# Kernel optimization log

Measured on AMD Instinct MI355X. Metric: run time of the kernel, lower is better.

## Reference

```python
import jax, jax.numpy as jnp
import numpy as np

K = 3          # kernel_size
G = 4          # num_groups


def conv_same(x, w, b):
    # x: [B,H,W,Cin], w: [kh,kw,Cin,Cout] (HWIO)
    return jax.lax.conv_general_dilated(
        x, w, (1, 1), 'SAME', dimension_numbers=('NHWC', 'HWIO', 'NHWC')) + b


def depthwise_same(x, w, b):
    # w: [kh,kw,1,C], feature_group_count=C -> depthwise conv
    c = x.shape[-1]
    return jax.lax.conv_general_dilated(
        x, w, (1, 1), 'SAME', dimension_numbers=('NHWC', 'HWIO', 'NHWC'),
        feature_group_count=c) + b


def kernel_grid(k, dtype):
    off = (k - 1) / 2.0
    lin = jnp.linspace(-off, off, k).astype(dtype)
    xg, yg = jnp.meshgrid(lin, lin)            # default 'xy' indexing, as in TF
    return jnp.stack([xg, yg], axis=-1).reshape(-1, 2)   # [K*K, 2]


def sample_with_offsets(x, offsets, k):
    # x: [B,H,W,C], offsets: [B,H,W,2*k*k]
    B, H, W, C = x.shape
    dt = x.dtype
    gy, gx = jnp.meshgrid(jnp.arange(H, dtype=dt), jnp.arange(W, dtype=dt), indexing='ij')
    grid = jnp.stack([gx, gy], axis=-1)[None, :, :, None, :]      # [1,H,W,1,2] (x,y)
    off = offsets.reshape(B, H, W, k * k, 2)
    kg = kernel_grid(k, dt).reshape(1, 1, 1, k * k, 2)
    loc = grid + kg + off                                          # [B,H,W,K2,2]
    lx = jnp.clip(loc[..., 0], 0.0, W - 1.0)
    ly = jnp.clip(loc[..., 1], 0.0, H - 1.0)
    x0 = jnp.clip(jnp.floor(lx), 0.0, W - 1.0)
    y0 = jnp.clip(jnp.floor(ly), 0.0, H - 1.0)
    x1 = jnp.clip(x0 + 1.0, 0.0, W - 1.0)
    y1 = jnp.clip(y0 + 1.0, 0.0, H - 1.0)
    # bilinear weights (computed with clipped corner coords, exactly as the TF code)
    wa = (x1 - lx) * (y1 - ly)
    wb = (x1 - lx) * (ly - y0)
    wc = (lx - x0) * (y1 - ly)
    wd = (lx - x0) * (ly - y0)
    flat = x.reshape(B, H * W, C)
    N = H * W * k * k

    def gather(yi, xi):
        idx = (yi * W + xi).astype(jnp.int32).reshape(B, N)
        return jnp.take_along_axis(flat, idx[..., None], axis=1)   # [B,N,C]

    Ia = gather(y0, x0)
    Ib = gather(y1, x0)
    Ic = gather(y0, x1)
    Id = gather(y1, x1)
    w_ = lambda w: w.reshape(B, N, 1)
    interp = w_(wa) * Ia + w_(wb) * Ib + w_(wc) * Ic + w_(wd) * Id  # [B,N,C]
    return interp.reshape(B, H, W, k * k * C)


def setup_inputs() -> dict:
    key = jax.random.key(0)
    ks = jax.random.split(key, 6)
    B, H, W, C = 4, 96, 96, 256
    Cg = C // G                 # 64
    K2C = K * K * Cg            # 576
    GF = 256 // G               # group_filters = 64
    x = jax.random.normal(ks[0], (B, H, W, C), dtype=jnp.float32)
    w_init = jax.random.normal(ks[1], (1, 1, C, C), dtype=jnp.float32) / np.sqrt(C)
    b_init = jnp.zeros((C,), dtype=jnp.float32)
    # offset conv weights small so learned offsets stay within a few pixels
    w_off = jax.random.normal(ks[2], (G, K, K, Cg, 2 * K * K), dtype=jnp.float32) * 0.01
    b_off = jnp.zeros((G, 2 * K * K), dtype=jnp.float32)
    w_dw = jax.random.normal(ks[3], (G, K, K, 1, K2C), dtype=jnp.float32) / 3.0
    b_dw = jnp.zeros((G, K2C), dtype=jnp.float32)
    w_pw = jax.random.normal(ks[4], (G, 1, 1, K2C, GF), dtype=jnp.float32) / np.sqrt(K2C)
    b_pw = jnp.zeros((G, GF), dtype=jnp.float32)
    return {"x": x, "w_init": w_init, "b_init": b_init,
            "w_off": w_off, "b_off": b_off,
            "w_dw": w_dw, "b_dw": b_dw,
            "w_pw": w_pw, "b_pw": b_pw}


def reference(x, w_init, b_init, w_off, b_off, w_dw, b_dw, w_pw, b_pw):
    B, H, W, C = x.shape
    Cg = C // G
    x = conv_same(x, w_init, b_init)                 # initial 1x1 conv, C->C
    xg = x.reshape(B, H, W, G, Cg)                   # channel split into groups
    outs = []
    for g in range(G):                               # small fixed group loop
        xi = xg[:, :, :, g, :]                       # [B,H,W,Cg]
        offsets = conv_same(xi, w_off[g], b_off[g])  # [B,H,W,2*K*K]
        sampled = sample_with_offsets(xi, offsets, K)  # [B,H,W,K*K*Cg]
        h = depthwise_same(sampled, w_dw[g], b_dw[g])
        outs.append(conv_same(h, w_pw[g], b_pw[g]))  # [B,H,W,group_filters]
    return jnp.concatenate(outs, axis=-1)            # [B,H,W,filters]
```

## Files before the change

### kernel.cpp

```cpp
#include <hip/hip_runtime.h>
#include <hip/hip_bf16.h>
#include <cstddef>

#define B_   4
#define H_   96
#define W_   96
#define C_   256
#define G_   4
#define CG   64
#define NPOS 9
#define KC   576
#define HW   (H_*W_)
#define NPIX (B_*H_*W_)

#define TM 4
#define TN 16
#define WROWS 6
#define WCOLS 18
#define WPOS  108

typedef float f32x4 __attribute__((ext_vector_type(4)));
typedef float f32x2 __attribute__((ext_vector_type(2)));
typedef short bf16x8 __attribute__((ext_vector_type(8)));

static __device__ __forceinline__ ushort f2bf(float f) {
    unsigned u = __float_as_uint(f);
    unsigned r = (u + 0x7fffu + ((u >> 16) & 1u)) >> 16;
    return (ushort)r;
}
static __device__ __forceinline__ float bf2f(ushort u) {
    return __uint_as_float(((unsigned)u) << 16);
}
static __device__ __forceinline__ f32x2 up2(unsigned u) {
    f32x2 f;
    f.x = __uint_as_float(u << 16);
    f.y = __uint_as_float(u & 0xFFFF0000u);
    return f;
}

__global__ void k_cvt_woffT(const float* __restrict__ w_off,
                            ushort* __restrict__ wtTh,
                            ushort* __restrict__ wtTl) {
    int idx = blockIdx.x * 256 + threadIdx.x;
    if (idx >= G_ * 32 * KC) return;
    int k  = idx % KC;
    int oc = (idx / KC) & 31;
    int g  = idx / (32 * KC);
    int p = k >> 6, c = k & 63;
    float v = 0.f;
    if (oc < 18) v = w_off[((size_t)(g * NPOS + p) * CG + c) * 18 + oc];
    ushort h = f2bf(v);
    wtTh[idx] = h;
    wtTl[idx] = f2bf(v - bf2f(h));
}

__global__ void k_cvt_wT_split(const float* __restrict__ w_init,
                               ushort* __restrict__ wTh,
                               ushort* __restrict__ wTl) {
    int idx = blockIdx.x * 256 + threadIdx.x;
    if (idx >= 256 * 256) return;
    int co = idx & 255, k = idx >> 8;
    float v = w_init[(size_t)k * 256 + co];
    ushort h = f2bf(v);
    wTh[(size_t)co * 256 + k] = h;
    wTl[(size_t)co * 256 + k] = f2bf(v - bf2f(h));
}

__global__ void k_cvt_wpwT(const float* __restrict__ w_pw,
                           ushort* __restrict__ wpwTh) {
    int idx = blockIdx.x * 256 + threadIdx.x;
    if (idx >= G_ * KC * CG) return;
    int f = idx & 63;
    int k = (idx >> 6) % KC;
    int g = idx / (KC * CG);
    wpwTh[((size_t)g * CG + f) * KC + k] = f2bf(w_pw[((size_t)g * KC + k) * CG + f]);
}

__global__ void __launch_bounds__(256) k_gemm_init_mfma(
        const float* __restrict__ x,
        const ushort* __restrict__ wTh, const ushort* __restrict__ wTl,
        const float* __restrict__ bias,
        ushort* __restrict__ yh, ushort* __restrict__ yl) {
    __shared__ __align__(16) ushort ath[64][72], atl[64][72];
    __shared__ __align__(16) ushort bth[64][72], btl[64][72];
    int t = threadIdx.x;
    int px0 = blockIdx.x * 64, n0 = blockIdx.y * 64;
    int r = t >> 2, seg = (t & 3) * 16;
    int lane = t & 63, wv = t >> 6;
    int hl = lane & 15, qv = lane >> 4;
    f32x4 acc[4] = {};
    for (int kk = 0; kk < C_; kk += 64) {
        {
            const float4* xs = (const float4*)(x + (size_t)(px0 + r) * C_ + kk + seg);
            ushort hbuf[16], lbuf[16];
            #pragma unroll
            for (int j = 0; j < 4; j++) {
                float4 v = xs[j];
                float vv[4] = {v.x, v.y, v.z, v.w};
                #pragma unroll
                for (int e2 = 0; e2 < 4; e2++) {
                    ushort h = f2bf(vv[e2]);
                    hbuf[j * 4 + e2] = h;
                    lbuf[j * 4 + e2] = f2bf(vv[e2] - bf2f(h));
                }
            }
            *(uint4*)&ath[r][seg]     = *(uint4*)&hbuf[0];
            *(uint4*)&ath[r][seg + 8] = *(uint4*)&hbuf[8];
            *(uint4*)&atl[r][seg]     = *(uint4*)&lbuf[0];
            *(uint4*)&atl[r][seg + 8] = *(uint4*)&lbuf[8];
        }
        {
            size_t woff = (size_t)(n0 + r) * C_ + kk + seg;
            const uint4* qh = (const uint4*)(wTh + woff);
            const uint4* ql = (const uint4*)(wTl + woff);
            uint4 c0 = qh[0], c1 = qh[1], d0 = ql[0], d1 = ql[1];
            *(uint4*)&bth[r][seg] = c0; *(uint4*)&bth[r][seg + 8] = c1;
            *(uint4*)&btl[r][seg] = d0; *(uint4*)&btl[r][seg + 8] = d1;
        }
        __syncthreads();
        #pragma unroll
        for (int ks = 0; ks < 2; ks++) {
            bf16x8 ah_ = *(const bf16x8*)&ath[wv * 16 + hl][ks * 32 + qv * 8];
            bf16x8 al_ = *(const bf16x8*)&atl[wv * 16 + hl][ks * 32 + qv * 8];
            #pragma unroll
            for (int cg = 0; cg < 4; cg++) {
                bf16x8 bh_ = *(const bf16x8*)&bth[cg * 16 + hl][ks * 32 + qv * 8];
                bf16x8 bl_ = *(const bf16x8*)&btl[cg * 16 + hl][ks * 32 + qv * 8];
                acc[cg] = __builtin_amdgcn_mfma_f32_16x16x32_bf16(ah_, bh_, acc[cg], 0, 0, 0);
                acc[cg] = __builtin_amdgcn_mfma_f32_16x16x32_bf16(ah_, bl_, acc[cg], 0, 0, 0);
                acc[cg] = __builtin_amdgcn_mfma_f32_16x16x32_bf16(al_, bh_, acc[cg], 0, 0, 0);
            }
        }
        __syncthreads();
    }
    #pragma unroll
    for (int cg = 0; cg < 4; cg++) {
        int col = n0 + cg * 16 + hl;
        float bb = bias[col];
        #pragma unroll
        for (int rg = 0; rg < 4; rg++) {
            int row = px0 + wv * 16 + qv * 4 + rg;
            float v = acc[cg][rg] + bb;
            ushort h = f2bf(v);
            yh[(size_t)row * C_ + col] = h;
            yl[(size_t)row * C_ + col] = f2bf(v - bf2f(h));
        }
    }
}

__global__ void __launch_bounds__(256) k_offconv_mfma(
        const ushort* __restrict__ yh, const ushort* __restrict__ yl,
        const ushort* __restrict__ wtTh, const ushort* __restrict__ wtTl,
        const float* __restrict__ b_off, float* __restrict__ off_all) {
    __shared__ __align__(16) ushort swh[WPOS][72], swl[WPOS][72];
    int g = blockIdx.y;
    int tile = blockIdx.x;
    int b = tile / 144; int trem = tile - b * 144;
    int r0 = (trem / 6) * TM;
    int c0 = (trem - (trem / 6) * 6) * TN;
    int t = threadIdx.x;
    int lane = t & 63, wv = t >> 6;
    int hl = lane & 15, qv = lane >> 4;
    const int bHW = b * HW;
    for (int i = t; i < WPOS * 32; i += 256) {
        int w = i >> 5, cq = i & 31;
        int wr = w / WCOLS, wc = w - wr * WCOLS;
        int ny = r0 - 1 + wr, nx = c0 - 1 + wc;
        unsigned vh = 0u, vl = 0u;
        if (((unsigned)ny < (unsigned)H_) && ((unsigned)nx < (unsigned)W_)) {
            size_t base = ((size_t)(bHW + ny * W_ + nx) * C_ + g * CG) >> 1;
            vh = ((const unsigned*)yh)[base + cq];
            vl = ((const unsigned*)yl)[base + cq];
        }
        *(unsigned*)&swh[w][cq * 2] = vh;
        *(unsigned*)&swl[w][cq * 2] = vl;
    }
    __syncthreads();
    f32x4 acc[2] = {};
    const ushort* Wh = wtTh + (size_t)g * 32 * KC;
    const ushort* Wl = wtTl + (size_t)g * 32 * KC;
    for (int p = 0; p < NPOS; p++) {
        int di = p / 3, dj = p - di * 3;
        int wbase = (wv + di) * WCOLS + dj + hl;
        #pragma unroll
        for (int ks = 0; ks < 2; ks++) {
            bf16x8 ah = *(const bf16x8*)&swh[wbase][ks * 32 + qv * 8];
            bf16x8 al = *(const bf16x8*)&swl[wbase][ks * 32 + qv * 8];
            #pragma unroll
            for (int cg = 0; cg < 2; cg++) {
                size_t wo = (size_t)(cg * 16 + hl) * KC + p * 64 + ks * 32 + qv * 8;
                bf16x8 bh = *(const bf16x8*)&Wh[wo];
                bf16x8 bl = *(const bf16x8*)&Wl[wo];
                acc[cg] = __builtin_amdgcn_mfma_f32_16x16x32_bf16(ah, bh, acc[cg], 0, 0, 0);
                acc[cg] = __builtin_amdgcn_mfma_f32_16x16x32_bf16(ah, bl, acc[cg], 0, 0, 0);
                acc[cg] = __builtin_amdgcn_mfma_f32_16x16x32_bf16(al, bh, acc[cg], 0, 0, 0);
                acc[cg] = __builtin_amdgcn_mfma_f32_16x16x32_bf16(al, bl, acc[cg], 0, 0, 0);
            }
        }
    }
    #pragma unroll
    for (int cg = 0; cg < 2; cg++) {
        int oc = cg * 16 + hl;
        if (oc < 18) {
            float bo = b_off[g * 18 + oc];
            #pragma unroll
            for (int rg = 0; rg < 4; rg++) {
                int pc = qv * 4 + rg;
                int px = bHW + (r0 + wv) * W_ + (c0 + pc);
                off_all[((size_t)g * NPIX + px) * 18 + oc] = acc[cg][rg] + bo;
            }
        }
    }
}

__global__ void __launch_bounds__(256) k_sample(
        const ushort* __restrict__ yh, const float* __restrict__ off_all,
        ushort* __restrict__ smp, int g0) {
    int gi = blockIdx.y;
    int g = g0 + gi;
    int t = threadIdx.x;
    int lane = t & 63, wv = t >> 6;
    int hs = lane >> 5;
    int cl = lane & 31;
    int w = blockIdx.x * 4 + wv;
    int s0 = w * 4;
    int p   = s0 / NPIX;
    int px0 = s0 - p * NPIX;
    int di = p / 3, dj = p - di * 3;
    const float* offg = off_all + (size_t)g * NPIX * 18;
    const unsigned* ybu = (const unsigned*)yh;
    unsigned* smpg = (unsigned*)smp + (size_t)gi * NPOS * NPIX * 32;
    #pragma unroll
    for (int q = 0; q < 2; q++) {
        int px = px0 + 2 * q + hs;
        float2 o2 = *(const float2*)&offg[(size_t)px * 18 + 2 * p];
        int b = px / HW; int r2 = px - b * HW;
        int yy = r2 / W_; int xx = r2 - yy * W_;
        float lx = (float)(xx + dj - 1) + o2.x;
        float ly = (float)(yy + di - 1) + o2.y;
        lx = fminf(fmaxf(lx, 0.f), (float)(W_ - 1));
        ly = fminf(fmaxf(ly, 0.f), (float)(H_ - 1));
        float x0f = floorf(lx), y0f = floorf(ly);
        float x1f = fminf(x0f + 1.f, (float)(W_ - 1));
        float y1f = fminf(y0f + 1.f, (float)(H_ - 1));
        float wa = (x1f - lx) * (y1f - ly);
        float wb = (x1f - lx) * (ly - y0f);
        float wc = (lx - x0f) * (y1f - ly);
        float wd = (lx - x0f) * (ly - y0f);
        int ix0 = (int)x0f, iy0 = (int)y0f, ix1 = (int)x1f, iy1 = (int)y1f;
        const unsigned* base = ybu + ((size_t)b * HW) * 128 + g * 32 + cl;
        f32x2 Ia = up2(base[(iy0 * W_ + ix0) * 128]);
        f32x2 Ib = up2(base[(iy1 * W_ + ix0) * 128]);
        f32x2 Ic = up2(base[(iy0 * W_ + ix1) * 128]);
        f32x2 Id = up2(base[(iy1 * W_ + ix1) * 128]);
        f32x2 v = wa * Ia + wb * Ib + wc * Ic + wd * Id;
        unsigned packed = (unsigned)f2bf(v.x) | ((unsigned)f2bf(v.y) << 16);
        smpg[((size_t)p * NPIX + px) * 32 + cl] = packed;
    }
}

__global__ void __launch_bounds__(256, 4) k_dwpw(
        const ushort* __restrict__ smp,
        const float* __restrict__ w_dw, const float* __restrict__ b_dw,
        const ushort* __restrict__ wpwTh, const float* __restrict__ b_pw,
        float* __restrict__ out, int g0) {
    __shared__ __align__(16) ushort swin[WPOS][64];
    __shared__ __align__(16) ushort ht [64][72];
    __shared__ __align__(16) ushort wt_[64][72];
    int gi = blockIdx.y;
    int g = g0 + gi;
    int bx = blockIdx.x;
    int tile = (bx & 7) * 72 + (bx >> 3);
    int b = tile / 144; int trem = tile - b * 144;
    int r0 = (trem / 6) * TM;
    int c0 = (trem - (trem / 6) * 6) * TN;
    int t = threadIdx.x;
    int lane = t & 63, wv = t >> 6;
    int hl = lane & 15, qv = lane >> 4;
    int rr = t >> 2, seg = (t & 3) * 16;
    const float* wdwg = w_dw + (size_t)g * NPOS * KC;
    const float* bdwg = b_dw + (size_t)g * KC;
    const ushort* wpwg = wpwTh + (size_t)g * CG * KC;
    const float* bpwg = b_pw + (size_t)g * CG;
    const int bHW = b * HW;
    int cp  = t & 31;
    int pxg = t >> 5;
    int pr  = pxg >> 1;
    int ph  = pxg & 1;

    int doff[4];
    int loff[4];
    #pragma unroll
    for (int k = 0; k < 4; k++) {
        int i = t + k * 256;
        doff[k] = -1; loff[k] = -1;
        if (i < WPOS * 8) {
            int w  = i >> 3;
            int cq = i & 7;
            int wr = w / WCOLS, wc = w - wr * WCOLS;
            loff[k] = w * 64 + cq * 8;
            int ny = r0 - 1 + wr, nx = c0 - 1 + wc;
            if (((unsigned)ny < (unsigned)H_) && ((unsigned)nx < (unsigned)W_))
                doff[k] = (bHW + ny * W_ + nx) * 64 + cq * 8;
        }
    }

    const size_t chunk_stride = (size_t)NPIX * 64;
    const ushort* smp_g = smp + (size_t)gi * NPOS * chunk_stride;
    ushort* swin_flat = &swin[0][0];

    f32x4 acc[4] = {};
    for (int p = 0; p < NPOS; p++) {
        {
            const uint4* s0 = (const uint4*)(wpwg + (size_t)rr * KC + p * 64 + seg);
            uint4 w0 = s0[0], w1 = s0[1];
            *(uint4*)&wt_[rr][seg]     = w0;
            *(uint4*)&wt_[rr][seg + 8] = w1;
        }
        const ushort* smp_p = smp_g + (size_t)p * chunk_stride;
        #pragma unroll
        for (int k = 0; k < 4; k++) {
            if (loff[k] >= 0) {
                uint4 v = make_uint4(0u, 0u, 0u, 0u);
                if (doff[k] >= 0) v = *(const uint4*)(smp_p + doff[k]);
                *(uint4*)(swin_flat + loff[k]) = v;
            }
        }
        __syncthreads();
        {
            f32x2 wd2[9];
            #pragma unroll
            for (int tap = 0; tap < 9; tap++) {
                float2 wv2 = *(const float2*)&wdwg[tap * KC + p * 64 + 2 * cp];
                wd2[tap] = {wv2.x, wv2.y};
            }
            float2 bdv = *(const float2*)&bdwg[p * 64 + 2 * cp];
            int rb0 = (pr + 0) * WCOLS + ph * 8;
            int rb1 = (pr + 1) * WCOLS + ph * 8;
            int rb2 = (pr + 2) * WCOLS + ph * 8;
            #define RD2(pos) up2(*(const unsigned*)&swin[pos][2 * cp])
            f32x2 a0 = RD2(rb0), e0 = RD2(rb0 + 1);
            f32x2 a1 = RD2(rb1), e1 = RD2(rb1 + 1);
            f32x2 a2 = RD2(rb2), e2 = RD2(rb2 + 1);
            #pragma unroll
            for (int c = 0; c < 8; c++) {
                f32x2 c0v = RD2(rb0 + c + 2);
                f32x2 c1v = RD2(rb1 + c + 2);
                f32x2 c2v = RD2(rb2 + c + 2);
                f32x2 hv = {bdv.x, bdv.y};
                hv = hv + a0 * wd2[0] + e0 * wd2[1] + c0v * wd2[2]
                        + a1 * wd2[3] + e1 * wd2[4] + c1v * wd2[5]
                        + a2 * wd2[6] + e2 * wd2[7] + c2v * wd2[8];
                int pxl = pr * 16 + ph * 8 + c;
                unsigned up = (unsigned)f2bf(hv.x) | ((unsigned)f2bf(hv.y) << 16);
                *(unsigned*)&ht[pxl][2 * cp] = up;
                a0 = e0; e0 = c0v; a1 = e1; e1 = c1v; a2 = e2; e2 = c2v;
            }
            #undef RD2
        }
        __syncthreads();
        #pragma unroll
        for (int ks = 0; ks < 2; ks++) {
            bf16x8 a = *(const bf16x8*)&ht[wv * 16 + hl][ks * 32 + qv * 8];
            #pragma unroll
            for (int cg = 0; cg < 4; cg++) {
                bf16x8 bfr = *(const bf16x8*)&wt_[cg * 16 + hl][ks * 32 + qv * 8];
                acc[cg] = __builtin_amdgcn_mfma_f32_16x16x32_bf16(a, bfr, acc[cg], 0, 0, 0);
            }
        }
        __syncthreads();
    }
    #pragma unroll
    for (int cg = 0; cg < 4; cg++) {
        int col = cg * 16 + hl;
        float bb = bpwg[col];
        #pragma unroll
        for (int rg = 0; rg < 4; rg++) {
            int pcol = qv * 4 + rg;
            int px = bHW + (r0 + wv) * W_ + (c0 + pcol);
            out[(size_t)px * C_ + g * CG + col] = acc[cg][rg] + bb;
        }
    }
}

extern "C" void kernel_launch(void* const* d_in, const int* in_sizes, int n_in,
                              void* d_out, int out_size, void* d_ws, size_t ws_size,
                              hipStream_t stream) {
    const float* x      = (const float*)d_in[0];
    const float* w_init = (const float*)d_in[1];
    const float* b_init = (const float*)d_in[2];
    const float* w_off  = (const float*)d_in[3];
    const float* b_off  = (const float*)d_in[4];
    const float* w_dw   = (const float*)d_in[5];
    const float* b_dw   = (const float*)d_in[6];
    const float* w_pw   = (const float*)d_in[7];
    const float* b_pw   = (const float*)d_in[8];
    float* out = (float*)d_out;

    float*  off_all = (float*)d_ws;
    ushort* yh      = (ushort*)(off_all + (size_t)G_ * NPIX * 18);
    ushort* yl      = yh + (size_t)NPIX * C_;
    ushort* wTh     = yl + (size_t)NPIX * C_;
    ushort* wTl     = wTh + 256 * 256;
    ushort* wpwTh   = wTl + 256 * 256;
    ushort* wtTh    = wpwTh + (size_t)G_ * KC * CG;
    ushort* wtTl    = wtTh + (size_t)G_ * 32 * KC;
    ushort* smp     = wtTl + (size_t)G_ * 32 * KC;

    size_t fixed_bytes = (size_t)((const char*)smp - (const char*)d_ws);
    size_t per_g = (size_t)NPOS * NPIX * CG * sizeof(ushort);
    int ng = 1;
    if      (ws_size >= fixed_bytes + 4 * per_g) ng = 4;
    else if (ws_size >= fixed_bytes + 2 * per_g) ng = 2;

    k_cvt_woffT<<<(G_ * 32 * KC + 255) / 256, 256, 0, stream>>>(w_off, wtTh, wtTl);
    k_cvt_wT_split<<<(256 * 256 + 255) / 256, 256, 0, stream>>>(w_init, wTh, wTl);
    k_cvt_wpwT<<<(G_ * KC * CG + 255) / 256, 256, 0, stream>>>(w_pw, wpwTh);
    k_gemm_init_mfma<<<dim3(NPIX / 64, C_ / 64), 256, 0, stream>>>(x, wTh, wTl,
                                                                   b_init, yh, yl);
    k_offconv_mfma<<<dim3(576, G_), 256, 0, stream>>>(yh, yl, wtTh, wtTl,
                                                      b_off, off_all);

    for (int g0 = 0; g0 < G_; g0 += ng) {
        k_sample<<<dim3(NPOS * NPIX / 16, ng), 256, 0, stream>>>(yh, off_all, smp, g0);
        k_dwpw<<<dim3(576, ng), 256, 0, stream>>>(smp, w_dw, b_dw, wpwTh,
                                                  b_pw, out, g0);
    }
}
```

Before: 300.5 us.

## Precompute bilinear weights and gather indices in a separate prep kernel per group

Moves the per-sample coordinate math (offset load, clamping, floor, bilinear weights, corner indices) out of k_sample into a new k_prep kernel that writes an 8-float table per sample. Before, each lane (32 per sample) redundantly did this math. It also drops the multi-group batching (ng=1..4 chosen by workspace size) and always processes one group at a time. The prep table costs extra global traffic plus one more launch per group, and the batching of groups into one launch is gone.

```diff
diff --git a/kernel.cpp b/kernel.cpp
--- a/kernel.cpp
+++ b/kernel.cpp
@@ -213,49 +213,62 @@
     }
 }
 
+__global__ void __launch_bounds__(256) k_prep(
+        const float* __restrict__ off_all, float* __restrict__ tab, int g) {
+    int s = blockIdx.x * 256 + threadIdx.x;
+    if (s >= NPOS * NPIX) return;
+    int p = s / NPIX;
+    int px = s - p * NPIX;
+    int di = p / 3, dj = p - di * 3;
+    int b = px / HW; int r2 = px - b * HW;
+    int yy = r2 / W_; int xx = r2 - yy * W_;
+    float2 o2 = *(const float2*)&off_all[((size_t)g * NPIX + px) * 18 + 2 * p];
+    float lx = (float)(xx + dj - 1) + o2.x;
+    float ly = (float)(yy + di - 1) + o2.y;
+    lx = fminf(fmaxf(lx, 0.f), (float)(W_ - 1));
+    ly = fminf(fmaxf(ly, 0.f), (float)(H_ - 1));
+    float x0f = floorf(lx), y0f = floorf(ly);
+    float x1f = fminf(x0f + 1.f, (float)(W_ - 1));
+    float y1f = fminf(y0f + 1.f, (float)(H_ - 1));
+    float wa = (x1f - lx) * (y1f - ly);
+    float wb = (x1f - lx) * (ly - y0f);
+    float wc = (lx - x0f) * (y1f - ly);
+    float wd = (lx - x0f) * (ly - y0f);
+    int ix0 = (int)x0f, iy0 = (int)y0f, ix1 = (int)x1f, iy1 = (int)y1f;
+    int base = (b * HW) * 128 + g * 32;
+    int ia = base + (iy0 * W_ + ix0) * 128;
+    int ib = base + (iy1 * W_ + ix0) * 128;
+    int ic = base + (iy0 * W_ + ix1) * 128;
+    int id = base + (iy1 * W_ + ix1) * 128;
+    float* tp8 = tab + (size_t)s * 8;
+    *(float4*)tp8 = make_float4(wa, wb, wc, wd);
+    int4 iv = make_int4(ia, ib, ic, id);
+    *(float4*)(tp8 + 4) = *(float4*)&iv;
+}
+
 __global__ void __launch_bounds__(256) k_sample(
-        const ushort* __restrict__ yh, const float* __restrict__ off_all,
-        ushort* __restrict__ smp, int g0) {
-    int gi = blockIdx.y;
-    int g = g0 + gi;
+        const ushort* __restrict__ yh, const float* __restrict__ tab,
+        ushort* __restrict__ smp) {
     int t = threadIdx.x;
     int lane = t & 63, wv = t >> 6;
     int hs = lane >> 5;
     int cl = lane & 31;
-    int w = blockIdx.x * 4 + wv;
-    int s0 = w * 4;
-    int p   = s0 / NPIX;
-    int px0 = s0 - p * NPIX;
-    int di = p / 3, dj = p - di * 3;
-    const float* offg = off_all + (size_t)g * NPIX * 18;
+    int s0 = (blockIdx.x * 4 + wv) * 4;
     const unsigned* ybu = (const unsigned*)yh;
-    unsigned* smpg = (unsigned*)smp + (size_t)gi * NPOS * NPIX * 32;
+    unsigned* smpg = (unsigned*)smp;
     #pragma unroll
     for (int q = 0; q < 2; q++) {
-        int px = px0 + 2 * q + hs;
-        float2 o2 = *(const float2*)&offg[(size_t)px * 18 + 2 * p];
-        int b = px / HW; int r2 = px - b * HW;
-        int yy = r2 / W_; int xx = r2 - yy * W_;
-        float lx = (float)(xx + dj - 1) + o2.x;
-        float ly = (float)(yy + di - 1) + o2.y;
-        lx = fminf(fmaxf(lx, 0.f), (float)(W_ - 1));
-        ly = fminf(fmaxf(ly, 0.f), (float)(H_ - 1));
-        float x0f = floorf(lx), y0f = floorf(ly);
-        float x1f = fminf(x0f + 1.f, (float)(W_ - 1));
-        float y1f = fminf(y0f + 1.f, (float)(H_ - 1));
-        float wa = (x1f - lx) * (y1f - ly);
-        float wb = (x1f - lx) * (ly - y0f);
-        float wc = (lx - x0f) * (y1f - ly);
-        float wd = (lx - x0f) * (ly - y0f);
-        int ix0 = (int)x0f, iy0 = (int)y0f, ix1 = (int)x1f, iy1 = (int)y1f;
-        const unsigned* base = ybu + ((size_t)b * HW) * 128 + g * 32 + cl;
-        f32x2 Ia = up2(base[(iy0 * W_ + ix0) * 128]);
-        f32x2 Ib = up2(base[(iy1 * W_ + ix0) * 128]);
-        f32x2 Ic = up2(base[(iy0 * W_ + ix1) * 128]);
-        f32x2 Id = up2(base[(iy1 * W_ + ix1) * 128]);
-        f32x2 v = wa * Ia + wb * Ib + wc * Ic + wd * Id;
+        int s = s0 + 2 * q + hs;
+        const float* e = tab + (size_t)s * 8;
+        float4 w4 = *(const float4*)e;
+        const int* ei = (const int*)(e + 4);
+        f32x2 Ia = up2(ybu[ei[0] + cl]);
+        f32x2 Ib = up2(ybu[ei[1] + cl]);
+        f32x2 Ic = up2(ybu[ei[2] + cl]);
+        f32x2 Id = up2(ybu[ei[3] + cl]);
+        f32x2 v = w4.x * Ia + w4.y * Ib + w4.z * Ic + w4.w * Id;
         unsigned packed = (unsigned)f2bf(v.x) | ((unsigned)f2bf(v.y) << 16);
-        smpg[((size_t)p * NPIX + px) * 32 + cl] = packed;
+        smpg[(size_t)s * 32 + cl] = packed;
     }
 }
 
@@ -263,12 +276,10 @@
         const ushort* __restrict__ smp,
         const float* __restrict__ w_dw, const float* __restrict__ b_dw,
         const ushort* __restrict__ wpwTh, const float* __restrict__ b_pw,
-        float* __restrict__ out, int g0) {
+        float* __restrict__ out, int g) {
     __shared__ __align__(16) ushort swin[WPOS][64];
     __shared__ __align__(16) ushort ht [64][72];
     __shared__ __align__(16) ushort wt_[64][72];
-    int gi = blockIdx.y;
-    int g = g0 + gi;
     int bx = blockIdx.x;
     int tile = (bx & 7) * 72 + (bx >> 3);
     int b = tile / 144; int trem = tile - b * 144;
@@ -306,7 +317,6 @@
     }
 
     const size_t chunk_stride = (size_t)NPIX * 64;
-    const ushort* smp_g = smp + (size_t)gi * NPOS * chunk_stride;
     ushort* swin_flat = &swin[0][0];
 
     f32x4 acc[4] = {};
@@ -317,7 +327,7 @@
             *(uint4*)&wt_[rr][seg]     = w0;
             *(uint4*)&wt_[rr][seg + 8] = w1;
         }
-        const ushort* smp_p = smp_g + (size_t)p * chunk_stride;
+        const ushort* smp_p = smp + (size_t)p * chunk_stride;
         #pragma unroll
         for (int k = 0; k < 4; k++) {
             if (loff[k] >= 0) {
@@ -405,13 +415,8 @@
     ushort* wpwTh   = wTl + 256 * 256;
     ushort* wtTh    = wpwTh + (size_t)G_ * KC * CG;
     ushort* wtTl    = wtTh + (size_t)G_ * 32 * KC;
-    ushort* smp     = wtTl + (size_t)G_ * 32 * KC;
-
-    size_t fixed_bytes = (size_t)((const char*)smp - (const char*)d_ws);
-    size_t per_g = (size_t)NPOS * NPIX * CG * sizeof(ushort);
-    int ng = 1;
-    if      (ws_size >= fixed_bytes + 4 * per_g) ng = 4;
-    else if (ws_size >= fixed_bytes + 2 * per_g) ng = 2;
+    float*  tab     = (float*)(wtTl + (size_t)G_ * 32 * KC);
+    ushort* smp     = (ushort*)(tab + (size_t)NPOS * NPIX * 8);
 
     k_cvt_woffT<<<(G_ * 32 * KC + 255) / 256, 256, 0, stream>>>(w_off, wtTh, wtTl);
     k_cvt_wT_split<<<(256 * 256 + 255) / 256, 256, 0, stream>>>(w_init, wTh, wTl);
@@ -421,9 +426,9 @@
     k_offconv_mfma<<<dim3(576, G_), 256, 0, stream>>>(yh, yl, wtTh, wtTl,
                                                       b_off, off_all);
 
-    for (int g0 = 0; g0 < G_; g0 += ng) {
-        k_sample<<<dim3(NPOS * NPIX / 16, ng), 256, 0, stream>>>(yh, off_all, smp, g0);
-        k_dwpw<<<dim3(576, ng), 256, 0, stream>>>(smp, w_dw, b_dw, wpwTh,
-                                                  b_pw, out, g0);
-    }
-}
+    for (int g = 0; g < G_; g++) {
+        k_prep<<<(NPOS * NPIX + 255) / 256, 256, 0, stream>>>(off_all, tab, g);
+        k_sample<<<NPOS * NPIX / 16, 256, 0, stream>>>(yh, tab, smp);
+        k_dwpw<<<576, 256, 0, stream>>>(smp, w_dw, b_dw, wpwTh, b_pw, out, g);
+    }
+}
```

New measurement: 343.0 us. 1.14x slower.
